# Kernel optimization log

Hardware: AMD Instinct MI355X
Metric: run time of the kernel (lower is better)

The kernel has to match this reference:

```python
import jax, jax.numpy as jnp
import numpy as np

L1, L2 = 16, 16            # lattice shape -> translation group
N_SYMM = L1 * L2           # 256 group elements
IN_FEATURES = 32
FEATURES = 64
BATCH = 16


def translation_table(l1, l2):
    """Product table pt[g, h] = index of g^{-1} h for the 2D translation group."""
    n = l1 * l2
    g = np.arange(n)
    a, b = g // l2, g % l2          # coords of g
    c, d = a, b                     # coords of h (same enumeration)
    pt = ((c[None, :] - a[:, None]) % l1) * l2 + ((d[None, :] - b[:, None]) % l2)
    return jnp.asarray(pt, dtype=jnp.int32)  # (n_symm, n_symm)


def setup_inputs() -> dict:
    key = jax.random.key(0)
    kx, kk, kb = jax.random.split(key, 3)
    x = jax.random.normal(kx, (BATCH, IN_FEATURES, N_SYMM), dtype=jnp.float32)
    # default_equivariant_initializer ~ lecun normal, fan_in = in_features * kernel_size
    scale = 1.0 / np.sqrt(IN_FEATURES * N_SYMM)
    kernel = scale * jax.random.normal(kk, (FEATURES, IN_FEATURES, N_SYMM), dtype=jnp.float32)
    bias = jnp.zeros((FEATURES,), dtype=jnp.float32)
    product_table = translation_table(L1, L2)
    return {"x": x, "kernel": kernel, "bias": bias, "product_table": product_table}


def reference(x, kernel, bias, product_table):
    # Expand kernel via group product table: K[f, i, g, h] = kernel[f, i, pt[g, h]]
    # (feature_group_count = 1, mask = None so unmask is identity, kernel_size = n_symm)
    K = jnp.take(kernel, product_table, axis=2)          # (F, I, S, S) -- 536 MB fp32
    # dot_general contracts x dims (in_features, n_symm) with K dims (I, first S)
    out = jnp.einsum('big,figh->bfh', x, K)              # (B, F, S)
    out = out + bias[:, None]                            # bias broadcast over group dim
    return out
```

## Files before the change

kernel.cpp:

```cpp
#include <hip/hip_runtime.h>

typedef unsigned short u16;
typedef unsigned int u32;
typedef __attribute__((ext_vector_type(8))) short bfx8;
typedef __attribute__((ext_vector_type(4))) float fx4;
typedef __attribute__((ext_vector_type(4))) u32 ux4;
typedef __attribute__((ext_vector_type(2))) u32 ux2;

__device__ inline u32 f2bf(float v) {
  u32 u = __builtin_bit_cast(u32, v);
  u = (u + 0x7fffu + ((u >> 16) & 1u)) >> 16;
  return u;
}

__global__ __launch_bounds__(512, 1) void eq_main(const float* __restrict__ xin,
                                                  const float* __restrict__ kin,
                                                  float* __restrict__ part) {
  __shared__ u16 As[32768];
  __shared__ u32 P4[2048];
  __shared__ u16 xraw[512];
  __shared__ float red[4 * 64 * 68];

  const int b = blockIdx.x & 15;
  const int ich = blockIdx.x >> 4;
  const int t = threadIdx.x;

  if (t < 128) {
    int iLoc = t >> 6, s4 = (t & 63) << 2;
    fx4 v = *(const fx4*)(xin + ((b << 5) + (ich << 1) + iLoc) * 256 + s4);
    ux2 p;
    p[0] = f2bf(v[0]) | (f2bf(v[1]) << 16);
    p[1] = f2bf(v[2]) | (f2bf(v[3]) << 16);
    *(ux2*)(xraw + iLoc * 256 + s4) = p;
  }

#pragma unroll
  for (int it = 0; it < 8; ++it) {
    int slot = it * 512 + t;
    int iLoc = slot >> 11;
    int f = (slot >> 5) & 63;
    int c = slot & 31;
    int cs = c ^ (f & 31);
    const float* src = kin + f * 8192 + ((ich << 1) + iLoc) * 256 + (cs << 3);
    fx4 v0 = *(const fx4*)src;
    fx4 v1 = *(const fx4*)(src + 4);
    ux4 p;
    p[0] = f2bf(v0[0]) | (f2bf(v0[1]) << 16);
    p[1] = f2bf(v0[2]) | (f2bf(v0[3]) << 16);
    p[2] = f2bf(v1[0]) | (f2bf(v1[1]) << 16);
    p[3] = f2bf(v1[2]) | (f2bf(v1[3]) << 16);
    *(ux4*)(As + slot * 8) = p;
  }
  __syncthreads();

  {
    int iLoc = t >> 8, e = t & 255;
    int r = e >> 4, par = (e >> 3) & 1, u0 = e & 7;
    const u16* xr = xraw + iLoc * 256 + (r << 4);
    ux4 q;
#pragma unroll
    for (int j = 0; j < 4; ++j) {
      int u = u0 + j;
      int c0 = (32 - 2 * u) & 15;
      u32 lo = xr[(c0 - par) & 15];
      u32 hi = xr[(c0 - par - 1) & 15];
      q[j] = lo | (hi << 16);
    }
    *(ux4*)(P4 + (t << 2)) = q;
  }
  __syncthreads();

  const int lane = t & 63;
  const int w = t >> 6;
  const int iLoc = w >> 2;
  const int wq = w & 3;
  const int n = lane & 15;
  const int quad = lane >> 4;
  const int s2_0 = (quad & 1) << 3;
  const int par = n & 1;
  const int u0 = ((s2_0 - n - par) & 15) >> 1;
  const int Pb4 = (iLoc << 10) + (par << 5) + (u0 << 2);
  const int s1q = quad >> 1;
  const u16* Aw = As + (iLoc << 14);

  fx4 acc[4][4];
#pragma unroll
  for (int a = 0; a < 4; ++a)
#pragma unroll
    for (int c = 0; c < 4; ++c) acc[a][c] = (fx4){0.f, 0.f, 0.f, 0.f};

#pragma unroll
  for (int kstep = 0; kstep < 8; ++kstep) {
    bfx8 af[4];
#pragma unroll
    for (int ft = 0; ft < 4; ++ft) {
      int f = (ft << 4) + n;
      int ch = ((kstep << 2) + quad) ^ (f & 31);
      af[ft] = *(const bfx8*)(Aw + f * 256 + ch * 8);
    }
    const int s1 = (kstep << 1) + s1q;
    bfx8 bfr[4];
#pragma unroll
    for (int ht = 0; ht < 4; ++ht) {
      int r = ((wq << 2) + ht - s1) & 15;
      bfr[ht] = __builtin_bit_cast(bfx8, *(const ux4*)(P4 + (r << 6) + Pb4));
    }
#pragma unroll
    for (int ft = 0; ft < 4; ++ft)
#pragma unroll
      for (int ht = 0; ht < 4; ++ht)
        acc[ft][ht] =
            __builtin_amdgcn_mfma_f32_16x16x32_bf16(af[ft], bfr[ht], acc[ft][ht], 0, 0, 0);
  }

  if (w >= 4) {
#pragma unroll
    for (int ft = 0; ft < 4; ++ft)
#pragma unroll
      for (int ht = 0; ht < 4; ++ht) {
        float* pr = &red[wq * 4352 + (ht * 16 + n) * 68 + (ft << 4) + (quad << 2)];
        *(fx4*)pr = acc[ft][ht];
      }
  }
  __syncthreads();
  if (w < 4) {
    float* pw = part + (((ich << 4) + b) << 14);
#pragma unroll
    for (int ft = 0; ft < 4; ++ft)
#pragma unroll
      for (int ht = 0; ht < 4; ++ht) {
        const float* pr = &red[wq * 4352 + (ht * 16 + n) * 68 + (ft << 4) + (quad << 2)];
        fx4 vv = *(const fx4*)pr;
        acc[ft][ht] = acc[ft][ht] + vv;
#pragma unroll
        for (int reg = 0; reg < 4; ++reg) {
          int f = (ft << 4) + (quad << 2) + reg;
          int h = (wq << 6) + (ht << 4) + n;
          pw[f * 256 + h] = acc[ft][ht][reg];
        }
      }
  }
}

__global__ __launch_bounds__(256) void eq_reduce(const float* __restrict__ part,
                                                 const float* __restrict__ bias,
                                                 float* __restrict__ out) {
  int o = (blockIdx.x * 256 + threadIdx.x) * 4;
  fx4 s = {0.f, 0.f, 0.f, 0.f};
#pragma unroll
  for (int i = 0; i < 16; ++i) s = s + *(const fx4*)(part + i * 262144 + o);
  float bv = bias[(o >> 8) & 63];
  s = s + (fx4){bv, bv, bv, bv};
  *(fx4*)(out + o) = s;
}

extern "C" void kernel_launch(void* const* d_in, const int* in_sizes, int n_in,
                              void* d_out, int out_size, void* d_ws, size_t ws_size,
                              hipStream_t stream) {
  (void)in_sizes; (void)n_in; (void)out_size; (void)ws_size;
  const float* x = (const float*)d_in[0];
  const float* k = (const float*)d_in[1];
  const float* bias = (const float*)d_in[2];
  float* part = (float*)d_ws;
  float* out = (float*)d_out;

  eq_main<<<256, 512, 0, stream>>>(x, k, part);
  eq_reduce<<<256, 256, 0, stream>>>(part, bias, out);
}
```

Before: 73.06 us.

## Replace partial-sum buffer and reduce kernel with atomic accumulation into output

The main kernel no longer writes per-channel-chunk partial sums to a workspace for a separate reduction pass. It atomically adds its results straight into the output, which a small zeroing kernel clears first, and the chunk-0 blocks add the bias. This removes the 16 MB partial-buffer write and read-back, at the cost of 16-way contended float atomics per output element, scalar atomic traffic, and nondeterministic summation order.

```diff
diff --git a/kernel.cpp b/kernel.cpp
--- a/kernel.cpp
+++ b/kernel.cpp
@@ -13,9 +13,15 @@
   return u;
 }
 
-__global__ __launch_bounds__(512, 1) void eq_main(const float* __restrict__ xin,
-                                                  const float* __restrict__ kin,
-                                                  float* __restrict__ part) {
+__global__ __launch_bounds__(256) void eq_zero(float* __restrict__ out) {
+  int o = (blockIdx.x * 256 + threadIdx.x) << 2;
+  *(fx4*)(out + o) = (fx4){0.f, 0.f, 0.f, 0.f};
+}
+
+__global__ __launch_bounds__(512, 1) void eq_fused(const float* __restrict__ xin,
+                                                   const float* __restrict__ kin,
+                                                   const float* __restrict__ bias,
+                                                   float* __restrict__ out) {
   __shared__ u16 As[32768];
   __shared__ u32 P4[2048];
   __shared__ u16 xraw[512];
@@ -124,46 +130,39 @@
   }
   __syncthreads();
   if (w < 4) {
-    float* pw = part + (((ich << 4) + b) << 14);
+    float* pw = out + (b << 14);
+    fx4 bv[4] = {(fx4){0.f, 0.f, 0.f, 0.f}, (fx4){0.f, 0.f, 0.f, 0.f},
+                 (fx4){0.f, 0.f, 0.f, 0.f}, (fx4){0.f, 0.f, 0.f, 0.f}};
+    if (ich == 0) {
+#pragma unroll
+      for (int ft = 0; ft < 4; ++ft)
+        bv[ft] = *(const fx4*)(bias + (ft << 4) + (quad << 2));
+    }
 #pragma unroll
     for (int ft = 0; ft < 4; ++ft)
 #pragma unroll
       for (int ht = 0; ht < 4; ++ht) {
         const float* pr = &red[wq * 4352 + (ht * 16 + n) * 68 + (ft << 4) + (quad << 2)];
         fx4 vv = *(const fx4*)pr;
-        acc[ft][ht] = acc[ft][ht] + vv;
+        fx4 s = acc[ft][ht] + vv + bv[ft];
+        int h = (wq << 6) + (ht << 4) + n;
 #pragma unroll
         for (int reg = 0; reg < 4; ++reg) {
           int f = (ft << 4) + (quad << 2) + reg;
-          int h = (wq << 6) + (ht << 4) + n;
-          pw[f * 256 + h] = acc[ft][ht][reg];
+          unsafeAtomicAdd(&pw[f * 256 + h], s[reg]);
         }
       }
   }
 }
 
-__global__ __launch_bounds__(256) void eq_reduce(const float* __restrict__ part,
-                                                 const float* __restrict__ bias,
-                                                 float* __restrict__ out) {
-  int o = (blockIdx.x * 256 + threadIdx.x) * 4;
-  fx4 s = {0.f, 0.f, 0.f, 0.f};
-#pragma unroll
-  for (int i = 0; i < 16; ++i) s = s + *(const fx4*)(part + i * 262144 + o);
-  float bv = bias[(o >> 8) & 63];
-  s = s + (fx4){bv, bv, bv, bv};
-  *(fx4*)(out + o) = s;
-}
-
 extern "C" void kernel_launch(void* const* d_in, const int* in_sizes, int n_in,
                               void* d_out, int out_size, void* d_ws, size_t ws_size,
                               hipStream_t stream) {
-  (void)in_sizes; (void)n_in; (void)out_size; (void)ws_size;
+  (void)in_sizes; (void)n_in; (void)out_size; (void)d_ws; (void)ws_size;
   const float* x = (const float*)d_in[0];
   const float* k = (const float*)d_in[1];
   const float* bias = (const float*)d_in[2];
-  float* part = (float*)d_ws;
   float* out = (float*)d_out;
-
-  eq_main<<<256, 512, 0, stream>>>(x, k, part);
-  eq_reduce<<<256, 256, 0, stream>>>(part, bias, out);
+  eq_zero<<<256, 256, 0, stream>>>(out);
+  eq_fused<<<256, 512, 0, stream>>>(x, k, bias, out);
 }
```

Measured after the change: 80.30 us. 1.1x slower.
